# Kernel tuning notes

Hardware: AMD Instinct MI355X
Metric: run time of the kernel (lower is better)

## Reference

```python
import jax, jax.numpy as jnp
import numpy as np

NEG_INF = -1e9  # matches tf mask value -1000000000.0
LEAKY_ALPHA = 0.2  # tf.nn.leaky_relu default


def setup_inputs() -> dict:
    key = jax.random.key(0)
    k1, k2, k3, k4 = jax.random.split(key, 4)
    B, N, F, U = 8, 2048, 128, 128
    X = jax.random.normal(k1, (B, N, F), dtype=jnp.float32)
    A = jax.random.randint(k2, (B, N, N), 0, 2, dtype=jnp.int32)
    W = jax.random.normal(k3, (F, U), dtype=jnp.float32) * 0.1
    a = jax.random.normal(k4, (2 * U, 1), dtype=jnp.float32) * 0.1
    return {"X": X, "A": A, "W": W, "a": a}


def reference(X, A, W, a):
    # H = X @ W : [B, N, U]
    H = jnp.einsum('bnf,fu->bnu', X, W)
    U = H.shape[-1]
    # Additive decomposition of the tile+concat: [H_i || H_j] @ a = H_i@a_src + H_j@a_dst
    a_src = a[:U, 0]   # [U]
    a_dst = a[U:, 0]   # [U]
    s = H @ a_src      # [B, N]
    t = H @ a_dst      # [B, N]
    e = s[:, :, None] + t[:, None, :]            # [B, N, N] pairwise logits
    e = jax.nn.leaky_relu(e, negative_slope=LEAKY_ALPHA)
    mask = jnp.where(A > 0, 0.0, NEG_INF).astype(e.dtype)
    attention = jax.nn.softmax(e + mask, axis=-1)  # [B, N, N]
    H_out = jnp.einsum('bij,bju->biu', attention, H)
    return jax.nn.relu(H_out)
```

## Files before the change

### kernel.cpp

```cpp
#include <hip/hip_runtime.h>
#include <hip/hip_bf16.h>


#define NEG_INF -1.0e9f

typedef __bf16 bf16x8 __attribute__((ext_vector_type(8)));
typedef unsigned short ushort8 __attribute__((ext_vector_type(8)));
typedef float f32x4 __attribute__((ext_vector_type(4)));

__device__ __forceinline__ unsigned short f2b(float x) {
    unsigned u = __builtin_bit_cast(unsigned, x);
    u += 0x7fffu + ((u >> 16) & 1u);
    return (unsigned short)(u >> 16);
}

__device__ __forceinline__ void gload_lds16(const void* g, void* l) {
    __builtin_amdgcn_global_load_lds(
        (const __attribute__((address_space(1))) void*)g,
        (__attribute__((address_space(3))) void*)l, 16, 0, 0);
}

__global__ __launch_bounds__(256) void k_h(const float* __restrict__ X,
                                           const float* __restrict__ W,
                                           const float* __restrict__ a,
                                           unsigned short* __restrict__ HT,
                                           float* __restrict__ sbuf,
                                           float* __restrict__ tbuf) {
    __shared__ unsigned short WT[128 * 136];

    const int tid  = threadIdx.x;
    const int w    = tid >> 6;
    const int lane = tid & 63;
    const int r    = lane & 15;
    const int cg   = lane >> 4;

    for (int i = tid; i < 16384; i += 256) {
        int u = i >> 7, f = i & 127;
        WT[u * 136 + f] = f2b(W[f * 128 + u]);
    }
    __syncthreads();

    const int row0 = blockIdx.x * 64 + w * 16;
    const int b    = row0 >> 11;
    const int n0   = row0 & 2047;
    const int arow = row0 + r;

    f32x4 acc[8] = {};

#pragma unroll
    for (int k0 = 0; k0 < 128; k0 += 32) {
        const float* xp = X + (size_t)arow * 128 + k0 + cg * 8;
        ushort8 xa;
#pragma unroll
        for (int j = 0; j < 8; j++) xa[j] = f2b(xp[j]);
        bf16x8 av = __builtin_bit_cast(bf16x8, xa);
#pragma unroll
        for (int ut = 0; ut < 8; ut++) {
            ushort8 wb = *(const ushort8*)(&WT[(ut * 16 + r) * 136 + k0 + cg * 8]);
            acc[ut] = __builtin_amdgcn_mfma_f32_16x16x32_bf16(
                av, __builtin_bit_cast(bf16x8, wb), acc[ut], 0, 0, 0);
        }
    }

    float sp[4] = {0.f, 0.f, 0.f, 0.f};
    float tp[4] = {0.f, 0.f, 0.f, 0.f};
#pragma unroll
    for (int ut = 0; ut < 8; ut++) {
        int u = ut * 16 + r;
        float as = a[u];
        float ad = a[128 + u];
#pragma unroll
        for (int reg = 0; reg < 4; reg++) {
            float h = acc[ut][reg];
            int nrow = n0 + cg * 4 + reg;
            HT[((size_t)b * 128 + u) * 2048 + nrow] = f2b(h);
            sp[reg] += h * as;
            tp[reg] += h * ad;
        }
    }
#pragma unroll
    for (int msk = 1; msk < 16; msk <<= 1) {
#pragma unroll
        for (int reg = 0; reg < 4; reg++) {
            sp[reg] += __shfl_xor(sp[reg], msk);
            tp[reg] += __shfl_xor(tp[reg], msk);
        }
    }
    if (r == 0) {
#pragma unroll
        for (int reg = 0; reg < 4; reg++) {
            int row = row0 + cg * 4 + reg;
            sbuf[row] = sp[reg];
            tbuf[row] = tp[reg];
        }
    }
}

__global__ __launch_bounds__(256, 2) void k_attn(const int* __restrict__ A,
                                                 const unsigned short* __restrict__ HT,
                                                 const float* __restrict__ sbuf,
                                                 const float* __restrict__ tbuf,
                                                 float* __restrict__ out) {
    __shared__ char smem[65536];
    __shared__ float dSm[4][32];

    const int tid  = threadIdx.x;
    const int jq   = tid >> 6;
    const int lane = tid & 63;
    const int r    = lane & 15;
    const int cg   = lane >> 4;
    const int bid  = blockIdx.x;
    const int b    = bid & 7;
    const int it   = bid >> 3;
    const int i0   = it * 32;
    const int rot  = it & 15;

    const int irow0 = i0 + r;
    const float s0 = sbuf[b * 2048 + irow0];
    const float s1 = sbuf[b * 2048 + irow0 + 16];
    const unsigned short* Hb = HT + ((size_t)b * 128) * 2048 + jq * 512;
    const int*   Aq0 = A    + ((size_t)(b * 2048 + irow0)) * 2048 + jq * 512 + cg * 8;
    const int*   Aq1 = Aq0 + 16 * 2048;
    const float* Tq  = tbuf + (size_t)b * 2048 + jq * 512 + cg * 8;

    const int srow = (lane >> 2);
    const int csrc = (lane & 3) ^ ((lane >> 2) & 3) ^ ((lane >> 4) & 3);
    char* const qbase = smem + jq * 16384;
    const unsigned short* src0 = Hb + (size_t)srow * 2048 + csrc * 8;
    const int rsl = ((r & 3) ^ ((r >> 2) & 3));

    f32x4 acc0[8] = {};
    f32x4 acc1[8] = {};
    float den0 = 0.f, den1 = 0.f;

    int4   aP0[2][2], aP1[2][2];
    float4 tP[2][2];
    {
        const int j0 = rot * 32;
        const int j1 = ((1 + rot) & 15) * 32;
        aP0[0][0] = *(const int4*)(Aq0 + j0);
        aP0[0][1] = *(const int4*)(Aq0 + j0 + 4);
        aP1[0][0] = *(const int4*)(Aq1 + j0);
        aP1[0][1] = *(const int4*)(Aq1 + j0 + 4);
        tP[0][0]  = *(const float4*)(Tq + j0);
        tP[0][1]  = *(const float4*)(Tq + j0 + 4);
        aP0[1][0] = *(const int4*)(Aq0 + j1);
        aP0[1][1] = *(const int4*)(Aq0 + j1 + 4);
        aP1[1][0] = *(const int4*)(Aq1 + j1);
        aP1[1][1] = *(const int4*)(Aq1 + j1 + 4);
        tP[1][0]  = *(const float4*)(Tq + j1);
        tP[1][1]  = *(const float4*)(Tq + j1 + 4);
#pragma unroll
        for (int i = 0; i < 8; i++)
            gload_lds16(src0 + (size_t)i * 16 * 2048 + j0,
                        qbase + i * 1024);
    }
    __syncthreads();

#pragma unroll
    for (int k = 0; k < 16; ++k) {
        const int p = k & 1;

        int4   ca0 = aP0[p][0], ca1 = aP0[p][1];
        int4   cb0 = aP1[p][0], cb1 = aP1[p][1];
        float4 ct0 = tP[p][0],  ct1 = tP[p][1];

        if (k < 15) {
            const int jn = ((k + 1 + rot) & 15) * 32;
            char* dst = qbase + (p ^ 1) * 8192;
#pragma unroll
            for (int i = 0; i < 8; i++)
                gload_lds16(src0 + (size_t)i * 16 * 2048 + jn,
                            dst + i * 1024);
        }
        if (k < 14) {
            const int ja = ((k + 2 + rot) & 15) * 32;
            aP0[p][0] = *(const int4*)(Aq0 + ja);
            aP0[p][1] = *(const int4*)(Aq0 + ja + 4);
            aP1[p][0] = *(const int4*)(Aq1 + ja);
            aP1[p][1] = *(const int4*)(Aq1 + ja + 4);
            tP[p][0]  = *(const float4*)(Tq + ja);
            tP[p][1]  = *(const float4*)(Tq + ja + 4);
        }

        float tv[8] = {ct0.x, ct0.y, ct0.z, ct0.w, ct1.x, ct1.y, ct1.z, ct1.w};
        int   a0i[8] = {ca0.x, ca0.y, ca0.z, ca0.w, ca1.x, ca1.y, ca1.z, ca1.w};
        int   a1i[8] = {cb0.x, cb0.y, cb0.z, cb0.w, cb1.x, cb1.y, cb1.z, cb1.w};
        bf16x8 pa0, pa1;
#pragma unroll
        for (int jj = 0; jj < 8; jj++) {
            float x0 = s0 + tv[jj];
            float e0 = fmaxf(x0, 0.2f * x0);
            float p0 = __expf(e0 - 16.0f);
            p0 = a0i[jj] > 0 ? p0 : 0.f;
            den0 += p0;
            pa0[jj] = (__bf16)p0;

            float x1 = s1 + tv[jj];
            float e1 = fmaxf(x1, 0.2f * x1);
            float p1 = __expf(e1 - 16.0f);
            p1 = a1i[jj] > 0 ? p1 : 0.f;
            den1 += p1;
            pa1[jj] = (__bf16)p1;
        }

        if (k < 14)      asm volatile("s_waitcnt vmcnt(14)" ::: "memory");
        else if (k < 15) asm volatile("s_waitcnt vmcnt(8)" ::: "memory");
        else             asm volatile("s_waitcnt vmcnt(0)" ::: "memory");
        __builtin_amdgcn_s_barrier();
        __builtin_amdgcn_sched_barrier(0);

        const char* buf = qbase + p * 8192;
#pragma unroll
        for (int ut = 0; ut < 8; ut++) {
            ushort8 hb = *(const ushort8*)(buf + (ut * 16 + r) * 64 +
                                           ((cg ^ rsl) * 16));
            bf16x8 hbv = __builtin_bit_cast(bf16x8, hb);
            acc0[ut] = __builtin_amdgcn_mfma_f32_16x16x32_bf16(pa0, hbv, acc0[ut], 0, 0, 0);
            acc1[ut] = __builtin_amdgcn_mfma_f32_16x16x32_bf16(pa1, hbv, acc1[ut], 0, 0, 0);
        }

        if (k < 15) {
            __builtin_amdgcn_s_barrier();
            __builtin_amdgcn_sched_barrier(0);
        }
    }

    den0 += __shfl_xor(den0, 16);
    den0 += __shfl_xor(den0, 32);
    den1 += __shfl_xor(den1, 16);
    den1 += __shfl_xor(den1, 32);

    __syncthreads();

    float* accS = (float*)smem;
    if (cg == 0) { dSm[jq][r] = den0; dSm[jq][16 + r] = den1; }
    if (jq != 0) {
        const int base = (jq - 1) * 32;
#pragma unroll
        for (int ut = 0; ut < 8; ut++)
#pragma unroll
            for (int reg = 0; reg < 4; reg++) {
                accS[(base + cg * 4 + reg) * 132 + ut * 16 + r]      = acc0[ut][reg];
                accS[(base + 16 + cg * 4 + reg) * 132 + ut * 16 + r] = acc1[ut][reg];
            }
    }
    __syncthreads();
    if (jq == 0) {
        float dinv0[4], dinv1[4];
#pragma unroll
        for (int reg = 0; reg < 4; reg++) {
            const int row0_ = cg * 4 + reg;
            const int row1_ = 16 + cg * 4 + reg;
            dinv0[reg] = 1.0f / (dSm[0][row0_] + dSm[1][row0_] +
                                 dSm[2][row0_] + dSm[3][row0_]);
            dinv1[reg] = 1.0f / (dSm[0][row1_] + dSm[1][row1_] +
                                 dSm[2][row1_] + dSm[3][row1_]);
        }
#pragma unroll
        for (int ut = 0; ut < 8; ut++) {
#pragma unroll
            for (int reg = 0; reg < 4; reg++) {
                const int lr0 = cg * 4 + reg;
                const int lr1 = 16 + cg * 4 + reg;
                float n0 = acc0[ut][reg]
                         + accS[(0 * 32 + lr0) * 132 + ut * 16 + r]
                         + accS[(1 * 32 + lr0) * 132 + ut * 16 + r]
                         + accS[(2 * 32 + lr0) * 132 + ut * 16 + r];
                float n1 = acc1[ut][reg]
                         + accS[(0 * 32 + lr1) * 132 + ut * 16 + r]
                         + accS[(1 * 32 + lr1) * 132 + ut * 16 + r]
                         + accS[(2 * 32 + lr1) * 132 + ut * 16 + r];
                out[((size_t)(b * 2048 + i0 + lr0)) * 128 + ut * 16 + r] =
                    fmaxf(n0 * dinv0[reg], 0.f);
                out[((size_t)(b * 2048 + i0 + lr1)) * 128 + ut * 16 + r] =
                    fmaxf(n1 * dinv1[reg], 0.f);
            }
        }
    }
}

extern "C" void kernel_launch(void* const* d_in, const int* in_sizes, int n_in,
                              void* d_out, int out_size, void* d_ws, size_t ws_size,
                              hipStream_t stream) {
    const float* X = (const float*)d_in[0];
    const int*   A = (const int*)d_in[1];
    const float* W = (const float*)d_in[2];
    const float* a = (const float*)d_in[3];
    float* out = (float*)d_out;

    char* ws = (char*)d_ws;
    float*          sb  = (float*)(ws);
    float*          tb  = (float*)(ws + 65536);
    unsigned short* HT  = (unsigned short*)(ws + 131072);

    k_h<<<dim3(256), dim3(256), 0, stream>>>(X, W, a, HT, sb, tb);
    k_attn<<<dim3(512), dim3(256), 0, stream>>>(A, HT, sb, tb, out);
}
```

Baseline: 60.01 us.

## Share H tiles across two row groups per block with 512-thread blocks

Each attention block now covers 64 query rows with 8 waves, two row groups per key quarter, and both groups share one LDS H tile. Each group loads half of that tile, so per-block H traffic into LDS is spread over twice the waves and total H reloads across the grid are halved. The grid shrinks from 512 to 256 blocks, which is about one block per CU and may reduce latency hiding. The epilogue reduction now runs in two serialized phases with extra barriers.

```diff
diff --git a/kernel.cpp b/kernel.cpp
--- a/kernel.cpp
+++ b/kernel.cpp
@@ -96,26 +96,28 @@
     }
 }
 
-__global__ __launch_bounds__(256, 2) void k_attn(const int* __restrict__ A,
-                                                 const unsigned short* __restrict__ HT,
-                                                 const float* __restrict__ sbuf,
-                                                 const float* __restrict__ tbuf,
-                                                 float* __restrict__ out) {
+__global__ __launch_bounds__(512) void k_attn(const int* __restrict__ A,
+                                              const unsigned short* __restrict__ HT,
+                                              const float* __restrict__ sbuf,
+                                              const float* __restrict__ tbuf,
+                                              float* __restrict__ out) {
     __shared__ char smem[65536];
-    __shared__ float dSm[4][32];
+    __shared__ float dSm[4][64];
 
     const int tid  = threadIdx.x;
-    const int jq   = tid >> 6;
+    const int w    = tid >> 6;
     const int lane = tid & 63;
     const int r    = lane & 15;
     const int cg   = lane >> 4;
+    const int jq   = w >> 1;
+    const int g    = w & 1;
     const int bid  = blockIdx.x;
     const int b    = bid & 7;
     const int it   = bid >> 3;
-    const int i0   = it * 32;
+    const int i0   = it * 64;
     const int rot  = it & 15;
 
-    const int irow0 = i0 + r;
+    const int irow0 = i0 + g * 32 + r;
     const float s0 = sbuf[b * 2048 + irow0];
     const float s1 = sbuf[b * 2048 + irow0 + 16];
     const unsigned short* Hb = HT + ((size_t)b * 128) * 2048 + jq * 512;
@@ -126,7 +128,7 @@
     const int srow = (lane >> 2);
     const int csrc = (lane & 3) ^ ((lane >> 2) & 3) ^ ((lane >> 4) & 3);
     char* const qbase = smem + jq * 16384;
-    const unsigned short* src0 = Hb + (size_t)srow * 2048 + csrc * 8;
+    const unsigned short* src0 = Hb + (size_t)(g * 64 + srow) * 2048 + csrc * 8;
     const int rsl = ((r & 3) ^ ((r >> 2) & 3));
 
     f32x4 acc0[8] = {};
@@ -151,9 +153,9 @@
         tP[1][0]  = *(const float4*)(Tq + j1);
         tP[1][1]  = *(const float4*)(Tq + j1 + 4);
 #pragma unroll
-        for (int i = 0; i < 8; i++)
+        for (int i = 0; i < 4; i++)
             gload_lds16(src0 + (size_t)i * 16 * 2048 + j0,
-                        qbase + i * 1024);
+                        qbase + (g * 4 + i) * 1024);
     }
     __syncthreads();
 
@@ -169,9 +171,9 @@
             const int jn = ((k + 1 + rot) & 15) * 32;
             char* dst = qbase + (p ^ 1) * 8192;
 #pragma unroll
-            for (int i = 0; i < 8; i++)
+            for (int i = 0; i < 4; i++)
                 gload_lds16(src0 + (size_t)i * 16 * 2048 + jn,
-                            dst + i * 1024);
+                            dst + (g * 4 + i) * 1024);
         }
         if (k < 14) {
             const int ja = ((k + 2 + rot) & 15) * 32;
@@ -204,8 +206,8 @@
             pa1[jj] = (__bf16)p1;
         }
 
-        if (k < 14)      asm volatile("s_waitcnt vmcnt(14)" ::: "memory");
-        else if (k < 15) asm volatile("s_waitcnt vmcnt(8)" ::: "memory");
+        if (k < 14)      asm volatile("s_waitcnt vmcnt(10)" ::: "memory");
+        else if (k < 15) asm volatile("s_waitcnt vmcnt(4)" ::: "memory");
         else             asm volatile("s_waitcnt vmcnt(0)" ::: "memory");
         __builtin_amdgcn_s_barrier();
         __builtin_amdgcn_sched_barrier(0);
@@ -233,48 +235,53 @@
 
     __syncthreads();
 
+    if (cg == 0) { dSm[jq][g * 32 + r] = den0; dSm[jq][g * 32 + 16 + r] = den1; }
+
     float* accS = (float*)smem;
-    if (cg == 0) { dSm[jq][r] = den0; dSm[jq][16 + r] = den1; }
-    if (jq != 0) {
-        const int base = (jq - 1) * 32;
-#pragma unroll
-        for (int ut = 0; ut < 8; ut++)
+#pragma unroll
+    for (int gg = 0; gg < 2; ++gg) {
+        __syncthreads();
+        if (g == gg && jq != 0) {
+            const int base = (jq - 1) * 32;
+#pragma unroll
+            for (int ut = 0; ut < 8; ut++)
+#pragma unroll
+                for (int reg = 0; reg < 4; reg++) {
+                    accS[(base + cg * 4 + reg) * 132 + ut * 16 + r]      = acc0[ut][reg];
+                    accS[(base + 16 + cg * 4 + reg) * 132 + ut * 16 + r] = acc1[ut][reg];
+                }
+        }
+        __syncthreads();
+        if (g == gg && jq == 0) {
+            float dinv0[4], dinv1[4];
 #pragma unroll
             for (int reg = 0; reg < 4; reg++) {
-                accS[(base + cg * 4 + reg) * 132 + ut * 16 + r]      = acc0[ut][reg];
-                accS[(base + 16 + cg * 4 + reg) * 132 + ut * 16 + r] = acc1[ut][reg];
+                const int row0_ = gg * 32 + cg * 4 + reg;
+                const int row1_ = gg * 32 + 16 + cg * 4 + reg;
+                dinv0[reg] = 1.0f / (dSm[0][row0_] + dSm[1][row0_] +
+                                     dSm[2][row0_] + dSm[3][row0_]);
+                dinv1[reg] = 1.0f / (dSm[0][row1_] + dSm[1][row1_] +
+                                     dSm[2][row1_] + dSm[3][row1_]);
             }
-    }
-    __syncthreads();
-    if (jq == 0) {
-        float dinv0[4], dinv1[4];
-#pragma unroll
-        for (int reg = 0; reg < 4; reg++) {
-            const int row0_ = cg * 4 + reg;
-            const int row1_ = 16 + cg * 4 + reg;
-            dinv0[reg] = 1.0f / (dSm[0][row0_] + dSm[1][row0_] +
-                                 dSm[2][row0_] + dSm[3][row0_]);
-            dinv1[reg] = 1.0f / (dSm[0][row1_] + dSm[1][row1_] +
-                                 dSm[2][row1_] + dSm[3][row1_]);
-        }
-#pragma unroll
-        for (int ut = 0; ut < 8; ut++) {
-#pragma unroll
-            for (int reg = 0; reg < 4; reg++) {
-                const int lr0 = cg * 4 + reg;
-                const int lr1 = 16 + cg * 4 + reg;
-                float n0 = acc0[ut][reg]
-                         + accS[(0 * 32 + lr0) * 132 + ut * 16 + r]
-                         + accS[(1 * 32 + lr0) * 132 + ut * 16 + r]
-                         + accS[(2 * 32 + lr0) * 132 + ut * 16 + r];
-                float n1 = acc1[ut][reg]
-                         + accS[(0 * 32 + lr1) * 132 + ut * 16 + r]
-                         + accS[(1 * 32 + lr1) * 132 + ut * 16 + r]
-                         + accS[(2 * 32 + lr1) * 132 + ut * 16 + r];
-                out[((size_t)(b * 2048 + i0 + lr0)) * 128 + ut * 16 + r] =
-                    fmaxf(n0 * dinv0[reg], 0.f);
-                out[((size_t)(b * 2048 + i0 + lr1)) * 128 + ut * 16 + r] =
-                    fmaxf(n1 * dinv1[reg], 0.f);
+#pragma unroll
+            for (int ut = 0; ut < 8; ut++) {
+#pragma unroll
+                for (int reg = 0; reg < 4; reg++) {
+                    const int lr0 = cg * 4 + reg;
+                    const int lr1 = 16 + cg * 4 + reg;
+                    float n0 = acc0[ut][reg]
+                             + accS[(0 * 32 + lr0) * 132 + ut * 16 + r]
+                             + accS[(1 * 32 + lr0) * 132 + ut * 16 + r]
+                             + accS[(2 * 32 + lr0) * 132 + ut * 16 + r];
+                    float n1 = acc1[ut][reg]
+                             + accS[(0 * 32 + lr1) * 132 + ut * 16 + r]
+                             + accS[(1 * 32 + lr1) * 132 + ut * 16 + r]
+                             + accS[(2 * 32 + lr1) * 132 + ut * 16 + r];
+                    out[((size_t)(b * 2048 + i0 + gg * 32 + lr0)) * 128 +
+                        ut * 16 + r] = fmaxf(n0 * dinv0[reg], 0.f);
+                    out[((size_t)(b * 2048 + i0 + gg * 32 + lr1)) * 128 +
+                        ut * 16 + r] = fmaxf(n1 * dinv1[reg], 0.f);
+                }
             }
         }
     }
@@ -295,5 +302,5 @@
     unsigned short* HT  = (unsigned short*)(ws + 131072);
 
     k_h<<<dim3(256), dim3(256), 0, stream>>>(X, W, a, HT, sb, tb);
-    k_attn<<<dim3(512), dim3(256), 0, stream>>>(A, HT, sb, tb, out);
-}
+    k_attn<<<dim3(256), dim3(512), 0, stream>>>(A, HT, sb, tb, out);
+}
```

Measured after the change: 59.26 us. Within noise of the previous version (-1.2%).

## Load H tiles directly from global into registers instead of LDS staging

Applied to the files above, without the earlier changes.

Removes the double-buffered global_load_lds staging of H tiles and the per-iteration barriers. Each lane now loads its MFMA B-operand fragments straight from global memory (L2-cached) into registers, and LDS shrinks to just the reduction buffer. This removes barrier synchronisation and LDS traffic and may raise occupancy. In exchange there are more uncoalesced 16-byte global loads, no explicit prefetch of H one step ahead, and load latency exposed right before the MFMAs.

```diff
diff --git a/kernel.cpp b/kernel.cpp
--- a/kernel.cpp
+++ b/kernel.cpp
@@ -12,12 +12,6 @@
     unsigned u = __builtin_bit_cast(unsigned, x);
     u += 0x7fffu + ((u >> 16) & 1u);
     return (unsigned short)(u >> 16);
-}
-
-__device__ __forceinline__ void gload_lds16(const void* g, void* l) {
-    __builtin_amdgcn_global_load_lds(
-        (const __attribute__((address_space(1))) void*)g,
-        (__attribute__((address_space(3))) void*)l, 16, 0, 0);
 }
 
 __global__ __launch_bounds__(256) void k_h(const float* __restrict__ X,
@@ -101,7 +95,7 @@
                                                  const float* __restrict__ sbuf,
                                                  const float* __restrict__ tbuf,
                                                  float* __restrict__ out) {
-    __shared__ char smem[65536];
+    __shared__ float accS[3 * 32 * 132];
     __shared__ float dSm[4][32];
 
     const int tid  = threadIdx.x;
@@ -119,15 +113,10 @@
     const float s0 = sbuf[b * 2048 + irow0];
     const float s1 = sbuf[b * 2048 + irow0 + 16];
     const unsigned short* Hb = HT + ((size_t)b * 128) * 2048 + jq * 512;
+    const unsigned short* Hrow = Hb + (size_t)r * 2048;
     const int*   Aq0 = A    + ((size_t)(b * 2048 + irow0)) * 2048 + jq * 512 + cg * 8;
     const int*   Aq1 = Aq0 + 16 * 2048;
     const float* Tq  = tbuf + (size_t)b * 2048 + jq * 512 + cg * 8;
-
-    const int srow = (lane >> 2);
-    const int csrc = (lane & 3) ^ ((lane >> 2) & 3) ^ ((lane >> 4) & 3);
-    char* const qbase = smem + jq * 16384;
-    const unsigned short* src0 = Hb + (size_t)srow * 2048 + csrc * 8;
-    const int rsl = ((r & 3) ^ ((r >> 2) & 3));
 
     f32x4 acc0[8] = {};
     f32x4 acc1[8] = {};
@@ -150,29 +139,16 @@
         aP1[1][1] = *(const int4*)(Aq1 + j1 + 4);
         tP[1][0]  = *(const float4*)(Tq + j1);
         tP[1][1]  = *(const float4*)(Tq + j1 + 4);
-#pragma unroll
-        for (int i = 0; i < 8; i++)
-            gload_lds16(src0 + (size_t)i * 16 * 2048 + j0,
-                        qbase + i * 1024);
-    }
-    __syncthreads();
+    }
 
 #pragma unroll
     for (int k = 0; k < 16; ++k) {
         const int p = k & 1;
+        const int jb = ((k + rot) & 15) * 32 + cg * 8;
 
         int4   ca0 = aP0[p][0], ca1 = aP0[p][1];
         int4   cb0 = aP1[p][0], cb1 = aP1[p][1];
         float4 ct0 = tP[p][0],  ct1 = tP[p][1];
-
-        if (k < 15) {
-            const int jn = ((k + 1 + rot) & 15) * 32;
-            char* dst = qbase + (p ^ 1) * 8192;
-#pragma unroll
-            for (int i = 0; i < 8; i++)
-                gload_lds16(src0 + (size_t)i * 16 * 2048 + jn,
-                            dst + i * 1024);
-        }
         if (k < 14) {
             const int ja = ((k + 2 + rot) & 15) * 32;
             aP0[p][0] = *(const int4*)(Aq0 + ja);
@@ -183,6 +159,11 @@
             tP[p][1]  = *(const float4*)(Tq + ja + 4);
         }
 
+        ushort8 hbv[8];
+#pragma unroll
+        for (int ut = 0; ut < 8; ut++)
+            hbv[ut] = *(const ushort8*)(Hrow + (size_t)(ut * 16) * 2048 + jb);
+
         float tv[8] = {ct0.x, ct0.y, ct0.z, ct0.w, ct1.x, ct1.y, ct1.z, ct1.w};
         int   a0i[8] = {ca0.x, ca0.y, ca0.z, ca0.w, ca1.x, ca1.y, ca1.z, ca1.w};
         int   a1i[8] = {cb0.x, cb0.y, cb0.z, cb0.w, cb1.x, cb1.y, cb1.z, cb1.w};
@@ -204,25 +185,11 @@
             pa1[jj] = (__bf16)p1;
         }
 
-        if (k < 14)      asm volatile("s_waitcnt vmcnt(14)" ::: "memory");
-        else if (k < 15) asm volatile("s_waitcnt vmcnt(8)" ::: "memory");
-        else             asm volatile("s_waitcnt vmcnt(0)" ::: "memory");
-        __builtin_amdgcn_s_barrier();
-        __builtin_amdgcn_sched_barrier(0);
-
-        const char* buf = qbase + p * 8192;
 #pragma unroll
         for (int ut = 0; ut < 8; ut++) {
-            ushort8 hb = *(const ushort8*)(buf + (ut * 16 + r) * 64 +
-                                           ((cg ^ rsl) * 16));
-            bf16x8 hbv = __builtin_bit_cast(bf16x8, hb);
-            acc0[ut] = __builtin_amdgcn_mfma_f32_16x16x32_bf16(pa0, hbv, acc0[ut], 0, 0, 0);
-            acc1[ut] = __builtin_amdgcn_mfma_f32_16x16x32_bf16(pa1, hbv, acc1[ut], 0, 0, 0);
-        }
-
-        if (k < 15) {
-            __builtin_amdgcn_s_barrier();
-            __builtin_amdgcn_sched_barrier(0);
+            bf16x8 hb = __builtin_bit_cast(bf16x8, hbv[ut]);
+            acc0[ut] = __builtin_amdgcn_mfma_f32_16x16x32_bf16(pa0, hb, acc0[ut], 0, 0, 0);
+            acc1[ut] = __builtin_amdgcn_mfma_f32_16x16x32_bf16(pa1, hb, acc1[ut], 0, 0, 0);
         }
     }
 
@@ -231,9 +198,6 @@
     den1 += __shfl_xor(den1, 16);
     den1 += __shfl_xor(den1, 32);
 
-    __syncthreads();
-
-    float* accS = (float*)smem;
     if (cg == 0) { dSm[jq][r] = den0; dSm[jq][16 + r] = den1; }
     if (jq != 0) {
         const int base = (jq - 1) * 32;
```

After: 66.88 us. +11.4%, slower.

## Warp-specialize attention kernel with producer waves loading H and packed mask

Applied to the files above, without the earlier changes.

Blocks grow to 512 threads. Four producer waves stream H tiles into a triple-buffered LDS stage and load the adjacency rows, packing each mask into bytes in shared memory. Four consumer waves read the packed mask bits, compute the probabilities and run the MFMAs, paced by s_barrier handshakes with the producers. This takes global-load latency and mask register pressure off the compute waves, at the cost of more LDS (about 96KB+), lower block occupancy, and a fragile hand-counted barrier protocol between the two roles.

```diff
diff --git a/kernel.cpp b/kernel.cpp
--- a/kernel.cpp
+++ b/kernel.cpp
@@ -96,121 +96,175 @@
     }
 }
 
-__global__ __launch_bounds__(256, 2) void k_attn(const int* __restrict__ A,
-                                                 const unsigned short* __restrict__ HT,
-                                                 const float* __restrict__ sbuf,
-                                                 const float* __restrict__ tbuf,
-                                                 float* __restrict__ out) {
-    __shared__ char smem[65536];
+__global__ __launch_bounds__(512) void k_attn(const int* __restrict__ A,
+                                              const unsigned short* __restrict__ HT,
+                                              const float* __restrict__ sbuf,
+                                              const float* __restrict__ tbuf,
+                                              float* __restrict__ out) {
+    __shared__ char smem[98304];
+    __shared__ unsigned int bitsS[4][2][256];
     __shared__ float dSm[4][32];
 
     const int tid  = threadIdx.x;
-    const int jq   = tid >> 6;
+    const int w    = tid >> 6;
     const int lane = tid & 63;
-    const int r    = lane & 15;
-    const int cg   = lane >> 4;
     const int bid  = blockIdx.x;
     const int b    = bid & 7;
     const int it   = bid >> 3;
     const int i0   = it * 32;
     const int rot  = it & 15;
-
+    const unsigned short* Hb = HT + ((size_t)b * 128) * 2048;
+
+    if (w >= 4) {
+        const int q = w - 4;
+        const int srow = lane >> 2;
+        const int csrc = (lane & 3) ^ ((lane >> 2) & 3) ^ ((lane >> 4) & 3);
+        const unsigned short* src0 = Hb + q * 512 + (size_t)srow * 2048 + csrc * 8;
+        char* const qstage = smem + q * 24576;
+        const int lr   = lane >> 1;
+        const int jsub = (lane & 1) * 16;
+        const int* Ap = A + ((size_t)(b * 2048 + i0 + lr)) * 2048 + q * 512 + jsub;
+
+        int4 aR[4][4];
+
+        {
+            const int j0 = rot * 32;
+            const int j1 = ((1 + rot) & 15) * 32;
+#pragma unroll
+            for (int i = 0; i < 8; i++)
+                gload_lds16(src0 + (size_t)i * 16 * 2048 + j0, qstage + i * 1024);
+#pragma unroll
+            for (int i = 0; i < 8; i++)
+                gload_lds16(src0 + (size_t)i * 16 * 2048 + j1, qstage + 8192 + i * 1024);
+#pragma unroll
+            for (int s = 0; s < 4; ++s) {
+                const int ja = ((s + rot) & 15) * 32;
+#pragma unroll
+                for (int c = 0; c < 4; ++c)
+                    aR[s][c] = *(const int4*)(Ap + ja + c * 4);
+            }
+            asm volatile("s_waitcnt vmcnt(0)" ::: "memory");
+            uint4 pk;
+            pk.x = (aR[0][0].x > 0 ? 1u : 0u) | (aR[0][0].y > 0 ? 1u : 0u) << 8 |
+                   (aR[0][0].z > 0 ? 1u : 0u) << 16 | (aR[0][0].w > 0 ? 1u : 0u) << 24;
+            pk.y = (aR[0][1].x > 0 ? 1u : 0u) | (aR[0][1].y > 0 ? 1u : 0u) << 8 |
+                   (aR[0][1].z > 0 ? 1u : 0u) << 16 | (aR[0][1].w > 0 ? 1u : 0u) << 24;
+            pk.z = (aR[0][2].x > 0 ? 1u : 0u) | (aR[0][2].y > 0 ? 1u : 0u) << 8 |
+                   (aR[0][2].z > 0 ? 1u : 0u) << 16 | (aR[0][2].w > 0 ? 1u : 0u) << 24;
+            pk.w = (aR[0][3].x > 0 ? 1u : 0u) | (aR[0][3].y > 0 ? 1u : 0u) << 8 |
+                   (aR[0][3].z > 0 ? 1u : 0u) << 16 | (aR[0][3].w > 0 ? 1u : 0u) << 24;
+            *(uint4*)(&bitsS[q][0][lr * 8 + (lane & 1) * 4]) = pk;
+            asm volatile("s_waitcnt lgkmcnt(0)" ::: "memory");
+        }
+        __builtin_amdgcn_s_barrier();
+        __builtin_amdgcn_sched_barrier(0);
+
+#pragma unroll
+        for (int k = 0; k < 16; ++k) {
+            if (k <= 13) {
+                const int jn = ((k + 2 + rot) & 15) * 32;
+                char* dst = qstage + ((k + 2) % 3) * 8192;
+#pragma unroll
+                for (int i = 0; i < 8; i++)
+                    gload_lds16(src0 + (size_t)i * 16 * 2048 + jn, dst + i * 1024);
+            }
+            if (k <= 11) {
+                const int ja = ((k + 4 + rot) & 15) * 32;
+#pragma unroll
+                for (int c = 0; c < 4; ++c)
+                    aR[k & 3][c] = *(const int4*)(Ap + ja + c * 4);
+            }
+            __builtin_amdgcn_sched_barrier(0);
+            if (k <= 11)      asm volatile("s_waitcnt vmcnt(16)" ::: "memory");
+            else if (k == 12) asm volatile("s_waitcnt vmcnt(12)" ::: "memory");
+            else if (k == 13) asm volatile("s_waitcnt vmcnt(8)"  ::: "memory");
+            else              asm volatile("s_waitcnt vmcnt(0)"  ::: "memory");
+            if (k <= 14) {
+                const int s = (k + 1) & 3;
+                uint4 pk;
+                pk.x = (aR[s][0].x > 0 ? 1u : 0u) | (aR[s][0].y > 0 ? 1u : 0u) << 8 |
+                       (aR[s][0].z > 0 ? 1u : 0u) << 16 | (aR[s][0].w > 0 ? 1u : 0u) << 24;
+                pk.y = (aR[s][1].x > 0 ? 1u : 0u) | (aR[s][1].y > 0 ? 1u : 0u) << 8 |
+                       (aR[s][1].z > 0 ? 1u : 0u) << 16 | (aR[s][1].w > 0 ? 1u : 0u) << 24;
+                pk.z = (aR[s][2].x > 0 ? 1u : 0u) | (aR[s][2].y > 0 ? 1u : 0u) << 8 |
+                       (aR[s][2].z > 0 ? 1u : 0u) << 16 | (aR[s][2].w > 0 ? 1u : 0u) << 24;
+                pk.w = (aR[s][3].x > 0 ? 1u : 0u) | (aR[s][3].y > 0 ? 1u : 0u) << 8 |
+                       (aR[s][3].z > 0 ? 1u : 0u) << 16 | (aR[s][3].w > 0 ? 1u : 0u) << 24;
+                *(uint4*)(&bitsS[q][(k + 1) & 1][lr * 8 + (lane & 1) * 4]) = pk;
+            }
+            asm volatile("s_waitcnt lgkmcnt(0)" ::: "memory");
+            if (k < 15) {
+                __builtin_amdgcn_s_barrier();
+                __builtin_amdgcn_sched_barrier(0);
+            }
+        }
+        __builtin_amdgcn_s_barrier();
+        __builtin_amdgcn_s_barrier();
+        return;
+    }
+
+    const int jq   = w;
+    const int r    = lane & 15;
+    const int cg   = lane >> 4;
     const int irow0 = i0 + r;
     const float s0 = sbuf[b * 2048 + irow0];
     const float s1 = sbuf[b * 2048 + irow0 + 16];
-    const unsigned short* Hb = HT + ((size_t)b * 128) * 2048 + jq * 512;
-    const int*   Aq0 = A    + ((size_t)(b * 2048 + irow0)) * 2048 + jq * 512 + cg * 8;
-    const int*   Aq1 = Aq0 + 16 * 2048;
-    const float* Tq  = tbuf + (size_t)b * 2048 + jq * 512 + cg * 8;
-
-    const int srow = (lane >> 2);
-    const int csrc = (lane & 3) ^ ((lane >> 2) & 3) ^ ((lane >> 4) & 3);
-    char* const qbase = smem + jq * 16384;
-    const unsigned short* src0 = Hb + (size_t)srow * 2048 + csrc * 8;
-    const int rsl = ((r & 3) ^ ((r >> 2) & 3));
+    const float* Tq = tbuf + (size_t)b * 2048 + jq * 512 + cg * 8;
+    char* const qstage = smem + jq * 24576;
+    const int rsl = (r & 3) ^ ((r >> 2) & 3);
 
     f32x4 acc0[8] = {};
     f32x4 acc1[8] = {};
     float den0 = 0.f, den1 = 0.f;
 
-    int4   aP0[2][2], aP1[2][2];
     float4 tP[2][2];
     {
         const int j0 = rot * 32;
         const int j1 = ((1 + rot) & 15) * 32;
-        aP0[0][0] = *(const int4*)(Aq0 + j0);
-        aP0[0][1] = *(const int4*)(Aq0 + j0 + 4);
-        aP1[0][0] = *(const int4*)(Aq1 + j0);
-        aP1[0][1] = *(const int4*)(Aq1 + j0 + 4);
-        tP[0][0]  = *(const float4*)(Tq + j0);
-        tP[0][1]  = *(const float4*)(Tq + j0 + 4);
-        aP0[1][0] = *(const int4*)(Aq0 + j1);
-        aP0[1][1] = *(const int4*)(Aq0 + j1 + 4);
-        aP1[1][0] = *(const int4*)(Aq1 + j1);
-        aP1[1][1] = *(const int4*)(Aq1 + j1 + 4);
-        tP[1][0]  = *(const float4*)(Tq + j1);
-        tP[1][1]  = *(const float4*)(Tq + j1 + 4);
-#pragma unroll
-        for (int i = 0; i < 8; i++)
-            gload_lds16(src0 + (size_t)i * 16 * 2048 + j0,
-                        qbase + i * 1024);
-    }
-    __syncthreads();
+        tP[0][0] = *(const float4*)(Tq + j0);
+        tP[0][1] = *(const float4*)(Tq + j0 + 4);
+        tP[1][0] = *(const float4*)(Tq + j1);
+        tP[1][1] = *(const float4*)(Tq + j1 + 4);
+    }
+    __builtin_amdgcn_s_barrier();
+    __builtin_amdgcn_sched_barrier(0);
 
 #pragma unroll
     for (int k = 0; k < 16; ++k) {
         const int p = k & 1;
-
-        int4   ca0 = aP0[p][0], ca1 = aP0[p][1];
-        int4   cb0 = aP1[p][0], cb1 = aP1[p][1];
-        float4 ct0 = tP[p][0],  ct1 = tP[p][1];
-
-        if (k < 15) {
-            const int jn = ((k + 1 + rot) & 15) * 32;
-            char* dst = qbase + (p ^ 1) * 8192;
-#pragma unroll
-            for (int i = 0; i < 8; i++)
-                gload_lds16(src0 + (size_t)i * 16 * 2048 + jn,
-                            dst + i * 1024);
-        }
+        float4 ct0 = tP[p][0], ct1 = tP[p][1];
         if (k < 14) {
             const int ja = ((k + 2 + rot) & 15) * 32;
-            aP0[p][0] = *(const int4*)(Aq0 + ja);
-            aP0[p][1] = *(const int4*)(Aq0 + ja + 4);
-            aP1[p][0] = *(const int4*)(Aq1 + ja);
-            aP1[p][1] = *(const int4*)(Aq1 + ja + 4);
-            tP[p][0]  = *(const float4*)(Tq + ja);
-            tP[p][1]  = *(const float4*)(Tq + ja + 4);
-        }
+            tP[p][0] = *(const float4*)(Tq + ja);
+            tP[p][1] = *(const float4*)(Tq + ja + 4);
+        }
+
+        const unsigned int* bb = &bitsS[jq][p][0];
+        uint2 m0 = *(const uint2*)(bb + r * 8 + cg * 2);
+        uint2 m1 = *(const uint2*)(bb + (r + 16) * 8 + cg * 2);
 
         float tv[8] = {ct0.x, ct0.y, ct0.z, ct0.w, ct1.x, ct1.y, ct1.z, ct1.w};
-        int   a0i[8] = {ca0.x, ca0.y, ca0.z, ca0.w, ca1.x, ca1.y, ca1.z, ca1.w};
-        int   a1i[8] = {cb0.x, cb0.y, cb0.z, cb0.w, cb1.x, cb1.y, cb1.z, cb1.w};
         bf16x8 pa0, pa1;
 #pragma unroll
         for (int jj = 0; jj < 8; jj++) {
+            const unsigned mb0 = ((jj < 4 ? m0.x : m0.y) >> ((jj & 3) * 8)) & 0xFFu;
+            const unsigned mb1 = ((jj < 4 ? m1.x : m1.y) >> ((jj & 3) * 8)) & 0xFFu;
             float x0 = s0 + tv[jj];
             float e0 = fmaxf(x0, 0.2f * x0);
             float p0 = __expf(e0 - 16.0f);
-            p0 = a0i[jj] > 0 ? p0 : 0.f;
+            p0 = mb0 ? p0 : 0.f;
             den0 += p0;
             pa0[jj] = (__bf16)p0;
 
             float x1 = s1 + tv[jj];
             float e1 = fmaxf(x1, 0.2f * x1);
             float p1 = __expf(e1 - 16.0f);
-            p1 = a1i[jj] > 0 ? p1 : 0.f;
+            p1 = mb1 ? p1 : 0.f;
             den1 += p1;
             pa1[jj] = (__bf16)p1;
         }
 
-        if (k < 14)      asm volatile("s_waitcnt vmcnt(14)" ::: "memory");
-        else if (k < 15) asm volatile("s_waitcnt vmcnt(8)" ::: "memory");
-        else             asm volatile("s_waitcnt vmcnt(0)" ::: "memory");
-        __builtin_amdgcn_s_barrier();
-        __builtin_amdgcn_sched_barrier(0);
-
-        const char* buf = qbase + p * 8192;
+        const char* buf = qstage + (k % 3) * 8192;
 #pragma unroll
         for (int ut = 0; ut < 8; ut++) {
             ushort8 hb = *(const ushort8*)(buf + (ut * 16 + r) * 64 +
@@ -231,7 +285,8 @@
     den1 += __shfl_xor(den1, 16);
     den1 += __shfl_xor(den1, 32);
 
-    __syncthreads();
+    __builtin_amdgcn_s_barrier();
+    __builtin_amdgcn_sched_barrier(0);
 
     float* accS = (float*)smem;
     if (cg == 0) { dSm[jq][r] = den0; dSm[jq][16 + r] = den1; }
@@ -245,7 +300,9 @@
                 accS[(base + 16 + cg * 4 + reg) * 132 + ut * 16 + r] = acc1[ut][reg];
             }
     }
-    __syncthreads();
+    asm volatile("s_waitcnt lgkmcnt(0)" ::: "memory");
+    __builtin_amdgcn_s_barrier();
+    __builtin_amdgcn_sched_barrier(0);
     if (jq == 0) {
         float dinv0[4], dinv1[4];
 #pragma unroll
@@ -295,5 +352,5 @@
     unsigned short* HT  = (unsigned short*)(ws + 131072);
 
     k_h<<<dim3(256), dim3(256), 0, stream>>>(X, W, a, HT, sb, tb);
-    k_attn<<<dim3(512), dim3(256), 0, stream>>>(A, HT, sb, tb, out);
-}
+    k_attn<<<dim3(512), dim3(512), 0, stream>>>(A, HT, sb, tb, out);
+}
```

New measurement: 70.21 us. 1.17x slower.
